# Optimization experiments

Hardware: AMD Instinct MI355X
Metric: run time of the kernel (lower is better)

## Reference

```python
import jax, jax.numpy as jnp
from jax import lax
import numpy as np


def _conv1d(x, w, b):
    # x: (N, C, L), w: (O, I, K), stride 2, padding 1 -> matches nn.Conv1d(k=4, s=2, p=1)
    y = lax.conv_general_dilated(x, w, window_strides=(2,), padding=[(1, 1)],
                                 dimension_numbers=('NCH', 'OIH', 'NCH'))
    return y + b[None, :, None]


def setup_inputs() -> dict:
    key = jax.random.key(0)
    k = jax.random.split(key, 6)
    B, C_in, T = 32, 256, 2048
    H, D, K_codes = 1024, 512, 1024
    s = 0.02
    return {
        'x': jax.random.normal(k[0], (B, C_in, T), dtype=jnp.float32),
        'w1': jax.random.normal(k[1], (H, C_in, 4), dtype=jnp.float32) * s,
        'b1': jnp.zeros((H,), dtype=jnp.float32),
        'w2': jax.random.normal(k[2], (D, H, 4), dtype=jnp.float32) * s,
        'b2': jnp.zeros((D,), dtype=jnp.float32),
        'codebook': jax.random.normal(k[3], (K_codes, D), dtype=jnp.float32) * s,
    }


def reference(x, w1, b1, w2, b2, codebook):
    z_e = _conv1d(jax.nn.relu(_conv1d(x, w1, b1)), w2, b2)  # (B, D, T/4)
    B, D, T = z_e.shape
    flat = z_e.transpose(0, 2, 1).reshape(-1, D)  # (B*T, D)
    # squared Euclidean distance; argmin identical to cdist(p=2) argmin
    d2 = (jnp.sum(flat * flat, axis=1, keepdims=True)
          - 2.0 * flat @ codebook.T
          + jnp.sum(codebook * codebook, axis=1)[None, :])  # (B*T, K)
    encoding_indices = jnp.argmin(d2, axis=1)  # (B*T,)
    # NOTE: faithful to the original .view(z_e.shape) (a raw reshape, no permute back)
    z_q = codebook[encoding_indices].reshape(B, D, T)
    return (z_q, encoding_indices, z_e)
```

## Files before the change

kernel.cpp:

```cpp
#include <hip/hip_runtime.h>
#include <hip/hip_bf16.h>

using f16x8 = __attribute__((ext_vector_type(8))) _Float16;
using f32x4 = __attribute__((ext_vector_type(4))) float;

union PackU { unsigned u; _Float16 h[2]; };

__device__ inline unsigned split_pack(float v) {
    _Float16 h0 = (_Float16)v;
    float r = (v - (float)h0) * 4096.0f;
    PackU p; p.h[0] = h0; p.h[1] = (_Float16)r;
    return p.u;
}

__global__ __launch_bounds__(256) void split_kernel(const float* __restrict__ src,
                                                    unsigned* __restrict__ dst, int n4) {
    int g = blockIdx.x * 256 + threadIdx.x;
    if (g >= n4) return;
    float4 v = reinterpret_cast<const float4*>(src)[g];
    uint4 o;
    o.x = split_pack(v.x); o.y = split_pack(v.y);
    o.z = split_pack(v.z); o.w = split_pack(v.w);
    reinterpret_cast<uint4*>(dst)[g] = o;
}

#define BMt 128
#define BNt 128
#define BKt 32

__global__ __launch_bounds__(256, 2) void mfma_gemm(
    const unsigned* __restrict__ Ap, const unsigned* __restrict__ Bp,
    const float* __restrict__ bias,
    unsigned* __restrict__ OutP, float* __restrict__ OutF,
    int M, int N, int KK, int Cc, int L, int Lout, int LoutSh,
    int gatherMode, int mode)
{
    __shared__ uint4 As4[BMt * 8];
    __shared__ uint4 Bs4[BNt * 8];

    const int tid = threadIdx.x;
    const int m0 = blockIdx.y * BMt;
    const int n0 = blockIdx.x * BNt;

    const int srow = tid >> 1;
    const int kh = tid & 1;
    const int am = m0 + srow;
    const int ab = am >> LoutSh;
    const int at = am & (Lout - 1);
    const unsigned* aprow = Ap + (size_t)ab * Cc * L;
    const int ai0 = 2 * at - 1;
    const unsigned* adir = Ap + (size_t)am * KK;
    const unsigned* brow = Bp + (size_t)(n0 + srow) * KK;

    const int lane = tid & 63;
    const int wv = tid >> 6;
    const int wr = wv >> 1, wc = wv & 1;
    const int l15 = lane & 15, lq = lane >> 4;

    f32x4 acc0[4][4] = {{{0.f}}};
    f32x4 acc1[4][4] = {{{0.f}}};

    for (int k0 = 0; k0 < KK; k0 += BKt) {
        uint4 pa[4], pb[4];
        if (gatherMode) {
            int cbase = (k0 >> 2) + kh * 4;
#pragma unroll
            for (int cl = 0; cl < 4; cl++) {
                const unsigned* base = aprow + (size_t)(cbase + cl) * L;
                unsigned q0 = 0, q3 = 0;
                if (ai0 >= 0) q0 = base[ai0];
                unsigned q1 = base[ai0 + 1];
                unsigned q2 = base[ai0 + 2];
                if (ai0 + 3 < L) q3 = base[ai0 + 3];
                pa[cl].x = q0; pa[cl].y = q1; pa[cl].z = q2; pa[cl].w = q3;
            }
        } else {
            const uint4* s = reinterpret_cast<const uint4*>(adir + k0 + kh * 16);
            pa[0] = s[0]; pa[1] = s[1]; pa[2] = s[2]; pa[3] = s[3];
        }
        {
            const uint4* s = reinterpret_cast<const uint4*>(brow + k0 + kh * 16);
            pb[0] = s[0]; pb[1] = s[1]; pb[2] = s[2]; pb[3] = s[3];
        }

        __syncthreads();

#pragma unroll
        for (int ch = 0; ch < 2; ch++) {
            uint4 w0, w1, v0, v1;
            unsigned* W0 = (unsigned*)&w0; unsigned* W1 = (unsigned*)&w1;
            unsigned* V0 = (unsigned*)&v0; unsigned* V1 = (unsigned*)&v1;
#pragma unroll
            for (int j = 0; j < 4; j++) {
                int e0 = ch * 8 + 2 * j, e1 = e0 + 1;
                unsigned lo = ((const unsigned*)&pa[e0 >> 2])[e0 & 3];
                unsigned hi = ((const unsigned*)&pa[e1 >> 2])[e1 & 3];
                W0[j] = (lo & 0xffffu) | (hi << 16);
                W1[j] = (lo >> 16) | (hi & 0xffff0000u);
                lo = ((const unsigned*)&pb[e0 >> 2])[e0 & 3];
                hi = ((const unsigned*)&pb[e1 >> 2])[e1 & 3];
                V0[j] = (lo & 0xffffu) | (hi << 16);
                V1[j] = (lo >> 16) | (hi & 0xffff0000u);
            }
            int kc = kh * 2 + ch;
            int sw = srow & 7;
            As4[srow * 8 + ((kc) ^ sw)] = w0;
            As4[srow * 8 + ((4 + kc) ^ sw)] = w1;
            Bs4[srow * 8 + ((kc) ^ sw)] = v0;
            Bs4[srow * 8 + ((4 + kc) ^ sw)] = v1;
        }

        __syncthreads();

        f16x8 a0f[4], a1f[4], b0f[4], b1f[4];
#pragma unroll
        for (int mf = 0; mf < 4; mf++) {
            int row = wr * 64 + mf * 16 + l15;
            int sw = row & 7;
            a0f[mf] = *reinterpret_cast<const f16x8*>(&As4[row * 8 + (lq ^ sw)]);
            a1f[mf] = *reinterpret_cast<const f16x8*>(&As4[row * 8 + ((4 + lq) ^ sw)]);
        }
#pragma unroll
        for (int nf = 0; nf < 4; nf++) {
            int row = wc * 64 + nf * 16 + l15;
            int sw = row & 7;
            b0f[nf] = *reinterpret_cast<const f16x8*>(&Bs4[row * 8 + (lq ^ sw)]);
            b1f[nf] = *reinterpret_cast<const f16x8*>(&Bs4[row * 8 + ((4 + lq) ^ sw)]);
        }
#pragma unroll
        for (int mf = 0; mf < 4; mf++)
#pragma unroll
            for (int nf = 0; nf < 4; nf++) {
                acc0[mf][nf] = __builtin_amdgcn_mfma_f32_16x16x32_f16(
                    a0f[mf], b0f[nf], acc0[mf][nf], 0, 0, 0);
                acc1[mf][nf] = __builtin_amdgcn_mfma_f32_16x16x32_f16(
                    a0f[mf], b1f[nf], acc1[mf][nf], 0, 0, 0);
                acc1[mf][nf] = __builtin_amdgcn_mfma_f32_16x16x32_f16(
                    a1f[mf], b0f[nf], acc1[mf][nf], 0, 0, 0);
            }
    }

    const float s12 = 1.0f / 4096.0f;
    const int LoutM = Lout - 1;

    if (mode == 2) {
#pragma unroll
        for (int mf = 0; mf < 4; mf++) {
            int mb = m0 + wr * 64 + mf * 16 + lq * 4;
#pragma unroll
            for (int nf = 0; nf < 4; nf++) {
                int n = n0 + wc * 64 + nf * 16 + l15;
#pragma unroll
                for (int r = 0; r < 4; r++) {
                    float v = acc0[mf][nf][r] + acc1[mf][nf][r] * s12;
                    OutF[(size_t)(mb + r) * N + n] = v;
                }
            }
        }
    } else if (mode == 0) {
#pragma unroll
        for (int mf = 0; mf < 4; mf++) {
            int mb = m0 + wr * 64 + mf * 16 + lq * 4;
            int b = mb >> LoutSh, t = mb & LoutM;
#pragma unroll
            for (int nf = 0; nf < 4; nf++) {
                int n = n0 + wc * 64 + nf * 16 + l15;
                float bv = bias[n];
                uint4 o;
                unsigned* O = (unsigned*)&o;
#pragma unroll
                for (int r = 0; r < 4; r++) {
                    float v = acc0[mf][nf][r] + acc1[mf][nf][r] * s12 + bv;
                    v = fmaxf(v, 0.f);
                    O[r] = split_pack(v);
                }
                *reinterpret_cast<uint4*>(&OutP[((size_t)b * N + n) * Lout + t]) = o;
            }
        }
    } else {
#pragma unroll
        for (int mf = 0; mf < 4; mf++) {
            int mb = m0 + wr * 64 + mf * 16 + lq * 4;
            int b = mb >> LoutSh, t = mb & LoutM;
#pragma unroll
            for (int nf = 0; nf < 4; nf++) {
                int n = n0 + wc * 64 + nf * 16 + l15;
                float bv = bias[n];
                float4 f;
                unsigned O[4];
#pragma unroll
                for (int r = 0; r < 4; r++) {
                    float v = acc0[mf][nf][r] + acc1[mf][nf][r] * s12 + bv;
                    ((float*)&f)[r] = v;
                    O[r] = split_pack(v);
                }
                *reinterpret_cast<float4*>(&OutF[((size_t)b * N + n) * Lout + t]) = f;
#pragma unroll
                for (int r = 0; r < 4; r++)
                    OutP[(size_t)(mb + r) * N + n] = O[r];
            }
        }
    }
}

__global__ __launch_bounds__(64) void cb_norm(const float* __restrict__ cb,
                                              float* __restrict__ cn2) {
    int n = blockIdx.x;
    int lane = threadIdx.x;
    float s = 0.f;
    for (int d = lane; d < 512; d += 64) {
        float v = cb[(size_t)n * 512 + d];
        s += v * v;
    }
#pragma unroll
    for (int off = 32; off; off >>= 1) s += __shfl_down(s, off);
    if (lane == 0) cn2[n] = s;
}

__global__ __launch_bounds__(256) void argmin_k(const float* __restrict__ S,
                                                const float* __restrict__ cn2,
                                                float* __restrict__ idxf,
                                                int* __restrict__ idxi, int rows) {
    int wid = threadIdx.x >> 6;
    int lane = threadIdx.x & 63;
    int r = blockIdx.x * 4 + wid;
    if (r >= rows) return;
    const float* srow = S + (size_t)r * 1024;
    float best = INFINITY;
    int bi = 0;
#pragma unroll
    for (int it = 0; it < 4; it++) {
        int nb = it * 256 + lane * 4;
        float4 s4 = *reinterpret_cast<const float4*>(&srow[nb]);
        float4 c4 = *reinterpret_cast<const float4*>(&cn2[nb]);
        float v;
        v = c4.x - 2.f * s4.x; if (v < best) { best = v; bi = nb + 0; }
        v = c4.y - 2.f * s4.y; if (v < best) { best = v; bi = nb + 1; }
        v = c4.z - 2.f * s4.z; if (v < best) { best = v; bi = nb + 2; }
        v = c4.w - 2.f * s4.w; if (v < best) { best = v; bi = nb + 3; }
    }
#pragma unroll
    for (int off = 32; off; off >>= 1) {
        float ov = __shfl_down(best, off);
        int oi = __shfl_down(bi, off);
        if (ov < best || (ov == best && oi < bi)) { best = ov; bi = oi; }
    }
    if (lane == 0) {
        idxf[r] = (float)bi;
        idxi[r] = bi;
    }
}

__global__ __launch_bounds__(256) void gather_k(const int* __restrict__ idx,
                                                const float* __restrict__ cb,
                                                float* __restrict__ zq, int total4) {
    int g = blockIdx.x * 256 + threadIdx.x;
    if (g >= total4) return;
    int r = g >> 7;
    int d4 = g & 127;
    int id = idx[r];
    *reinterpret_cast<float4*>(&zq[(size_t)r * 512 + (size_t)d4 * 4]) =
        *reinterpret_cast<const float4*>(&cb[(size_t)id * 512 + (size_t)d4 * 4]);
}

extern "C" void kernel_launch(void* const* d_in, const int* in_sizes, int n_in,
                              void* d_out, int out_size, void* d_ws, size_t ws_size,
                              hipStream_t stream) {
    const float* x  = (const float*)d_in[0];
    const float* w1 = (const float*)d_in[1];
    const float* b1 = (const float*)d_in[2];
    const float* w2 = (const float*)d_in[3];
    const float* b2 = (const float*)d_in[4];
    const float* cb = (const float*)d_in[5];
    float* out = (float*)d_out;

    const int B = 32, Cin = 256, T = 2048, H = 1024, D = 512, Kc = 1024;
    const int T1 = 1024, T2 = 512;

    float* zq_out  = out;
    float* idx_out = out + (size_t)B * T2 * D;
    float* ze_out  = idx_out + (size_t)B * T2;

    unsigned* w1p = (unsigned*)d_ws;
    unsigned* w2p = w1p + (size_t)H * Cin * 4;
    unsigned* cbp = w2p + (size_t)D * H * 4;
    float* cn2    = (float*)(cbp + (size_t)Kc * D);
    int* idx_ws   = (int*)(cn2 + Kc);
    unsigned* dyn = (unsigned*)(idx_ws + B * T2);

    size_t fixed_u32 = (size_t)H * Cin * 4 + (size_t)D * H * 4 + (size_t)Kc * D
                       + Kc + (size_t)B * T2 + 256;
    int NB = 32;
    while (NB > 1 &&
           (fixed_u32 + (size_t)NB * ((size_t)Cin * T + (size_t)H * T1 + (size_t)T2 * D))
               * 4 > ws_size)
        NB >>= 1;

    unsigned* xp = dyn;
    unsigned* hp = xp + (size_t)NB * Cin * T;
    unsigned* zp = hp + (size_t)NB * H * T1;
    float* S = (float*)hp;

    split_kernel<<<(H * Cin * 4 / 4 + 255) / 256, 256, 0, stream>>>(w1, w1p, H * Cin * 4 / 4);
    split_kernel<<<(D * H * 4 / 4 + 255) / 256, 256, 0, stream>>>(w2, w2p, D * H * 4 / 4);
    split_kernel<<<(Kc * D / 4 + 255) / 256, 256, 0, stream>>>(cb, cbp, Kc * D / 4);
    cb_norm<<<Kc, 64, 0, stream>>>(cb, cn2);

    for (int b0 = 0; b0 < B; b0 += NB) {
        int nb = (B - b0 < NB) ? (B - b0) : NB;

        split_kernel<<<(nb * Cin * T / 4 + 255) / 256, 256, 0, stream>>>(
            x + (size_t)b0 * Cin * T, xp, nb * Cin * T / 4);

        mfma_gemm<<<dim3(H / BNt, nb * T1 / BMt), 256, 0, stream>>>(
            xp, w1p, b1, hp, nullptr,
            nb * T1, H, Cin * 4, Cin, T, T1, 10, 1, 0);

        mfma_gemm<<<dim3(D / BNt, nb * T2 / BMt), 256, 0, stream>>>(
            hp, w2p, b2, zp, ze_out + (size_t)b0 * D * T2,
            nb * T2, D, H * 4, H, T1, T2, 9, 1, 1);

        mfma_gemm<<<dim3(Kc / BNt, nb * T2 / BMt), 256, 0, stream>>>(
            zp, cbp, nullptr, nullptr, S,
            nb * T2, Kc, D, D, T2, T2, 9, 0, 2);

        argmin_k<<<(nb * T2 + 3) / 4, 256, 0, stream>>>(
            S, cn2, idx_out + (size_t)b0 * T2, idx_ws, nb * T2);

        gather_k<<<(nb * T2 * D / 4 + 255) / 256, 256, 0, stream>>>(
            idx_ws, cb, zq_out + (size_t)b0 * T2 * D, nb * T2 * D / 4);
    }
}
```

Baseline: 598.6 us.

## Split fp16 hi/lo into separate planes and prefetch next K tile

Stores the fp16 high and residual parts in separate planar buffers instead of interleaved 32-bit pairs. This lets the GEMM load tiles with wide vector loads and use byte permutes for the conv gather instead of per-element shuffling. It also prefetches the next K tile into registers while MFMAs run, changes the LDS swizzle, and reorders weight taps in split_w. The cost is extra workspace bookkeeping and more complex gather logic with edge masks, which risks subtle correctness issues.

```diff
diff --git a/kernel.cpp b/kernel.cpp
--- a/kernel.cpp
+++ b/kernel.cpp
@@ -3,54 +3,81 @@
 
 using f16x8 = __attribute__((ext_vector_type(8))) _Float16;
 using f32x4 = __attribute__((ext_vector_type(4))) float;
-
-union PackU { unsigned u; _Float16 h[2]; };
-
-__device__ inline unsigned split_pack(float v) {
-    _Float16 h0 = (_Float16)v;
-    float r = (v - (float)h0) * 4096.0f;
-    PackU p; p.h[0] = h0; p.h[1] = (_Float16)r;
-    return p.u;
-}
-
-__global__ __launch_bounds__(256) void split_kernel(const float* __restrict__ src,
-                                                    unsigned* __restrict__ dst, int n4) {
+typedef unsigned uint4a __attribute__((ext_vector_type(4), aligned(4)));
+
+__device__ inline void sp2(float v, unsigned short& h0, unsigned short& h1) {
+    _Float16 a = (_Float16)v;
+    float r = (v - (float)a) * 4096.0f;
+    _Float16 b = (_Float16)r;
+    union { _Float16 f; unsigned short u; } c0, c1;
+    c0.f = a; c1.f = b;
+    h0 = c0.u; h1 = c1.u;
+}
+
+__global__ __launch_bounds__(256) void split_planes(const float* __restrict__ src,
+        ushort* __restrict__ p0, ushort* __restrict__ p1, int n4) {
     int g = blockIdx.x * 256 + threadIdx.x;
     if (g >= n4) return;
     float4 v = reinterpret_cast<const float4*>(src)[g];
-    uint4 o;
-    o.x = split_pack(v.x); o.y = split_pack(v.y);
-    o.z = split_pack(v.z); o.w = split_pack(v.w);
-    reinterpret_cast<uint4*>(dst)[g] = o;
-}
-
-#define BMt 128
-#define BNt 128
-#define BKt 32
+    ushort4 a, b;
+    sp2(v.x, a.x, b.x); sp2(v.y, a.y, b.y);
+    sp2(v.z, a.z, b.z); sp2(v.w, a.w, b.w);
+    *reinterpret_cast<ushort4*>(&p0[(size_t)g * 4]) = a;
+    *reinterpret_cast<ushort4*>(&p1[(size_t)g * 4]) = b;
+}
+
+__global__ __launch_bounds__(256) void split_w(const float* __restrict__ w,
+        ushort* __restrict__ p0, ushort* __restrict__ p1, int total) {
+    int g = blockIdx.x * 256 + threadIdx.x;
+    if (g >= total) return;
+    float4 v = reinterpret_cast<const float4*>(w)[g];
+    ushort4 a, b;
+    sp2(v.y, a.x, b.x);
+    sp2(v.z, a.y, b.y);
+    sp2(v.x, a.z, b.z);
+    sp2(v.w, a.w, b.w);
+    *reinterpret_cast<ushort4*>(&p0[(size_t)g * 4]) = a;
+    *reinterpret_cast<ushort4*>(&p1[(size_t)g * 4]) = b;
+}
 
 __global__ __launch_bounds__(256, 2) void mfma_gemm(
-    const unsigned* __restrict__ Ap, const unsigned* __restrict__ Bp,
+    const ushort* __restrict__ A0, const ushort* __restrict__ A1,
+    const ushort* __restrict__ B0, const ushort* __restrict__ B1,
     const float* __restrict__ bias,
-    unsigned* __restrict__ OutP, float* __restrict__ OutF,
+    ushort* __restrict__ OP0, ushort* __restrict__ OP1,
+    float* __restrict__ OutF,
     int M, int N, int KK, int Cc, int L, int Lout, int LoutSh,
     int gatherMode, int mode)
 {
-    __shared__ uint4 As4[BMt * 8];
-    __shared__ uint4 Bs4[BNt * 8];
+    __shared__ uint4 As4[128 * 8];
+    __shared__ uint4 Bs4[128 * 8];
 
     const int tid = threadIdx.x;
-    const int m0 = blockIdx.y * BMt;
-    const int n0 = blockIdx.x * BNt;
+    const int m0 = blockIdx.y * 128;
+    const int n0 = blockIdx.x * 128;
 
     const int srow = tid >> 1;
     const int kh = tid & 1;
+    const int sw_s = (srow ^ (srow >> 3)) & 7;
+
     const int am = m0 + srow;
     const int ab = am >> LoutSh;
     const int at = am & (Lout - 1);
-    const unsigned* aprow = Ap + (size_t)ab * Cc * L;
-    const int ai0 = 2 * at - 1;
-    const unsigned* adir = Ap + (size_t)am * KK;
-    const unsigned* brow = Bp + (size_t)(n0 + srow) * KK;
+
+    const ushort* ag0 = nullptr;
+    const ushort* ag1 = nullptr;
+    const ushort* ad = nullptr;
+    unsigned bmask = 0xffffffffu;
+    if (gatherMode) {
+        long long off = (long long)ab * Cc * L + 2 * at - 2;
+        ag0 = A0 + off;
+        ag1 = A1 + off;
+        if (at == 0) bmask &= 0xffff0000u;
+        if (at == Lout - 1) bmask &= 0x0000ffffu;
+    } else {
+        ad = (kh ? A1 : A0) + (size_t)am * KK;
+    }
+    const ushort* bd = (kh ? B1 : B0) + (size_t)(n0 + srow) * KK;
 
     const int lane = tid & 63;
     const int wv = tid >> 6;
@@ -60,84 +87,85 @@
     f32x4 acc0[4][4] = {{{0.f}}};
     f32x4 acc1[4][4] = {{{0.f}}};
 
-    for (int k0 = 0; k0 < KK; k0 += BKt) {
-        uint4 pa[4], pb[4];
+    uint4 aw[4], bw[4];
+
+    auto loadA = [&](int k0) {
         if (gatherMode) {
-            int cbase = (k0 >> 2) + kh * 4;
-#pragma unroll
-            for (int cl = 0; cl < 4; cl++) {
-                const unsigned* base = aprow + (size_t)(cbase + cl) * L;
-                unsigned q0 = 0, q3 = 0;
-                if (ai0 >= 0) q0 = base[ai0];
-                unsigned q1 = base[ai0 + 1];
-                unsigned q2 = base[ai0 + 2];
-                if (ai0 + 3 < L) q3 = base[ai0 + 3];
-                pa[cl].x = q0; pa[cl].y = q1; pa[cl].z = q2; pa[cl].w = q3;
+            int cb_ = (k0 >> 2) + kh * 4;
+#pragma unroll
+            for (int q = 0; q < 2; q++) {
+                const ushort* l0 = ag0 + (size_t)(cb_ + 2 * q) * L;
+                const ushort* l1 = ag0 + (size_t)(cb_ + 2 * q + 1) * L;
+                const ushort* l2 = ag1 + (size_t)(cb_ + 2 * q) * L;
+                const ushort* l3 = ag1 + (size_t)(cb_ + 2 * q + 1) * L;
+                uint4a x0 = *(const uint4a*)l0;
+                uint4a x1 = *(const uint4a*)l1;
+                uint4a x2 = *(const uint4a*)l2;
+                uint4a x3 = *(const uint4a*)l3;
+                aw[q].x = x0.y;
+                aw[q].y = __builtin_amdgcn_perm(x0.z, x0.x, 0x05040302u) & bmask;
+                aw[q].z = x1.y;
+                aw[q].w = __builtin_amdgcn_perm(x1.z, x1.x, 0x05040302u) & bmask;
+                aw[2 + q].x = x2.y;
+                aw[2 + q].y = __builtin_amdgcn_perm(x2.z, x2.x, 0x05040302u) & bmask;
+                aw[2 + q].z = x3.y;
+                aw[2 + q].w = __builtin_amdgcn_perm(x3.z, x3.x, 0x05040302u) & bmask;
             }
         } else {
-            const uint4* s = reinterpret_cast<const uint4*>(adir + k0 + kh * 16);
-            pa[0] = s[0]; pa[1] = s[1]; pa[2] = s[2]; pa[3] = s[3];
-        }
-        {
-            const uint4* s = reinterpret_cast<const uint4*>(brow + k0 + kh * 16);
-            pb[0] = s[0]; pb[1] = s[1]; pb[2] = s[2]; pb[3] = s[3];
-        }
-
+#pragma unroll
+            for (int q = 0; q < 4; q++)
+                aw[q] = *reinterpret_cast<const uint4*>(ad + k0 + q * 8);
+        }
+    };
+    auto loadB = [&](int k0) {
+#pragma unroll
+        for (int q = 0; q < 4; q++)
+            bw[q] = *reinterpret_cast<const uint4*>(bd + k0 + q * 8);
+    };
+
+    loadA(0);
+    loadB(0);
+
+    for (int k0 = 0; k0 < KK; k0 += 32) {
         __syncthreads();
-
-#pragma unroll
-        for (int ch = 0; ch < 2; ch++) {
-            uint4 w0, w1, v0, v1;
-            unsigned* W0 = (unsigned*)&w0; unsigned* W1 = (unsigned*)&w1;
-            unsigned* V0 = (unsigned*)&v0; unsigned* V1 = (unsigned*)&v1;
-#pragma unroll
-            for (int j = 0; j < 4; j++) {
-                int e0 = ch * 8 + 2 * j, e1 = e0 + 1;
-                unsigned lo = ((const unsigned*)&pa[e0 >> 2])[e0 & 3];
-                unsigned hi = ((const unsigned*)&pa[e1 >> 2])[e1 & 3];
-                W0[j] = (lo & 0xffffu) | (hi << 16);
-                W1[j] = (lo >> 16) | (hi & 0xffff0000u);
-                lo = ((const unsigned*)&pb[e0 >> 2])[e0 & 3];
-                hi = ((const unsigned*)&pb[e1 >> 2])[e1 & 3];
-                V0[j] = (lo & 0xffffu) | (hi << 16);
-                V1[j] = (lo >> 16) | (hi & 0xffff0000u);
-            }
-            int kc = kh * 2 + ch;
-            int sw = srow & 7;
-            As4[srow * 8 + ((kc) ^ sw)] = w0;
-            As4[srow * 8 + ((4 + kc) ^ sw)] = w1;
-            Bs4[srow * 8 + ((kc) ^ sw)] = v0;
-            Bs4[srow * 8 + ((4 + kc) ^ sw)] = v1;
-        }
-
+        if (gatherMode) {
+            As4[srow * 8 + ((2 * kh + 0) ^ sw_s)] = aw[0];
+            As4[srow * 8 + ((2 * kh + 1) ^ sw_s)] = aw[1];
+            As4[srow * 8 + ((4 + 2 * kh + 0) ^ sw_s)] = aw[2];
+            As4[srow * 8 + ((4 + 2 * kh + 1) ^ sw_s)] = aw[3];
+        } else {
+#pragma unroll
+            for (int q = 0; q < 4; q++)
+                As4[srow * 8 + ((4 * kh + q) ^ sw_s)] = aw[q];
+        }
+#pragma unroll
+        for (int q = 0; q < 4; q++)
+            Bs4[srow * 8 + ((4 * kh + q) ^ sw_s)] = bw[q];
         __syncthreads();
 
-        f16x8 a0f[4], a1f[4], b0f[4], b1f[4];
+        if (k0 + 32 < KK) { loadA(k0 + 32); loadB(k0 + 32); }
+
+        f16x8 a0f[4], a1f[4];
 #pragma unroll
         for (int mf = 0; mf < 4; mf++) {
             int row = wr * 64 + mf * 16 + l15;
-            int sw = row & 7;
+            int sw = (row ^ (row >> 3)) & 7;
             a0f[mf] = *reinterpret_cast<const f16x8*>(&As4[row * 8 + (lq ^ sw)]);
             a1f[mf] = *reinterpret_cast<const f16x8*>(&As4[row * 8 + ((4 + lq) ^ sw)]);
         }
 #pragma unroll
         for (int nf = 0; nf < 4; nf++) {
             int row = wc * 64 + nf * 16 + l15;
-            int sw = row & 7;
-            b0f[nf] = *reinterpret_cast<const f16x8*>(&Bs4[row * 8 + (lq ^ sw)]);
-            b1f[nf] = *reinterpret_cast<const f16x8*>(&Bs4[row * 8 + ((4 + lq) ^ sw)]);
-        }
-#pragma unroll
-        for (int mf = 0; mf < 4; mf++)
-#pragma unroll
-            for (int nf = 0; nf < 4; nf++) {
-                acc0[mf][nf] = __builtin_amdgcn_mfma_f32_16x16x32_f16(
-                    a0f[mf], b0f[nf], acc0[mf][nf], 0, 0, 0);
-                acc1[mf][nf] = __builtin_amdgcn_mfma_f32_16x16x32_f16(
-                    a0f[mf], b1f[nf], acc1[mf][nf], 0, 0, 0);
-                acc1[mf][nf] = __builtin_amdgcn_mfma_f32_16x16x32_f16(
-                    a1f[mf], b0f[nf], acc1[mf][nf], 0, 0, 0);
-            }
+            int sw = (row ^ (row >> 3)) & 7;
+            f16x8 b0f = *reinterpret_cast<const f16x8*>(&Bs4[row * 8 + (lq ^ sw)]);
+            f16x8 b1f = *reinterpret_cast<const f16x8*>(&Bs4[row * 8 + ((4 + lq) ^ sw)]);
+#pragma unroll
+            for (int mf = 0; mf < 4; mf++) {
+                acc0[mf][nf] = __builtin_amdgcn_mfma_f32_16x16x32_f16(a0f[mf], b0f, acc0[mf][nf], 0, 0, 0);
+                acc1[mf][nf] = __builtin_amdgcn_mfma_f32_16x16x32_f16(a0f[mf], b1f, acc1[mf][nf], 0, 0, 0);
+                acc1[mf][nf] = __builtin_amdgcn_mfma_f32_16x16x32_f16(a1f[mf], b0f, acc1[mf][nf], 0, 0, 0);
+            }
+        }
     }
 
     const float s12 = 1.0f / 4096.0f;
@@ -151,10 +179,8 @@
             for (int nf = 0; nf < 4; nf++) {
                 int n = n0 + wc * 64 + nf * 16 + l15;
 #pragma unroll
-                for (int r = 0; r < 4; r++) {
-                    float v = acc0[mf][nf][r] + acc1[mf][nf][r] * s12;
-                    OutF[(size_t)(mb + r) * N + n] = v;
-                }
+                for (int r = 0; r < 4; r++)
+                    OutF[(size_t)(mb + r) * N + n] = acc0[mf][nf][r] + acc1[mf][nf][r] * s12;
             }
         }
     } else if (mode == 0) {
@@ -166,15 +192,15 @@
             for (int nf = 0; nf < 4; nf++) {
                 int n = n0 + wc * 64 + nf * 16 + l15;
                 float bv = bias[n];
-                uint4 o;
-                unsigned* O = (unsigned*)&o;
-#pragma unroll
-                for (int r = 0; r < 4; r++) {
-                    float v = acc0[mf][nf][r] + acc1[mf][nf][r] * s12 + bv;
-                    v = fmaxf(v, 0.f);
-                    O[r] = split_pack(v);
-                }
-                *reinterpret_cast<uint4*>(&OutP[((size_t)b * N + n) * Lout + t]) = o;
+                ushort4 o0, o1;
+                float v;
+                v = fmaxf(acc0[mf][nf][0] + acc1[mf][nf][0] * s12 + bv, 0.f); sp2(v, o0.x, o1.x);
+                v = fmaxf(acc0[mf][nf][1] + acc1[mf][nf][1] * s12 + bv, 0.f); sp2(v, o0.y, o1.y);
+                v = fmaxf(acc0[mf][nf][2] + acc1[mf][nf][2] * s12 + bv, 0.f); sp2(v, o0.z, o1.z);
+                v = fmaxf(acc0[mf][nf][3] + acc1[mf][nf][3] * s12 + bv, 0.f); sp2(v, o0.w, o1.w);
+                size_t base = ((size_t)b * N + n) * Lout + t;
+                *reinterpret_cast<ushort4*>(&OP0[base]) = o0;
+                *reinterpret_cast<ushort4*>(&OP1[base]) = o1;
             }
         }
     } else {
@@ -187,17 +213,19 @@
                 int n = n0 + wc * 64 + nf * 16 + l15;
                 float bv = bias[n];
                 float4 f;
-                unsigned O[4];
+                unsigned short h0[4], h1[4];
 #pragma unroll
                 for (int r = 0; r < 4; r++) {
                     float v = acc0[mf][nf][r] + acc1[mf][nf][r] * s12 + bv;
                     ((float*)&f)[r] = v;
-                    O[r] = split_pack(v);
+                    sp2(v, h0[r], h1[r]);
                 }
                 *reinterpret_cast<float4*>(&OutF[((size_t)b * N + n) * Lout + t]) = f;
 #pragma unroll
-                for (int r = 0; r < 4; r++)
-                    OutP[(size_t)(mb + r) * N + n] = O[r];
+                for (int r = 0; r < 4; r++) {
+                    OP0[(size_t)(mb + r) * N + n] = h0[r];
+                    OP1[(size_t)(mb + r) * N + n] = h1[r];
+                }
             }
         }
     }
@@ -281,48 +309,60 @@
     float* idx_out = out + (size_t)B * T2 * D;
     float* ze_out  = idx_out + (size_t)B * T2;
 
-    unsigned* w1p = (unsigned*)d_ws;
-    unsigned* w2p = w1p + (size_t)H * Cin * 4;
-    unsigned* cbp = w2p + (size_t)D * H * 4;
-    float* cn2    = (float*)(cbp + (size_t)Kc * D);
-    int* idx_ws   = (int*)(cn2 + Kc);
-    unsigned* dyn = (unsigned*)(idx_ws + B * T2);
-
-    size_t fixed_u32 = (size_t)H * Cin * 4 + (size_t)D * H * 4 + (size_t)Kc * D
-                       + Kc + (size_t)B * T2 + 256;
+    ushort* wsb = (ushort*)d_ws;
+    size_t cur = 32;
+    auto alloc16 = [&](size_t n) {
+        ushort* p = wsb + cur;
+        cur += (n + 31) & ~(size_t)31;
+        return p;
+    };
+
+    ushort* w1p0 = alloc16((size_t)H * Cin * 4);
+    ushort* w1p1 = alloc16((size_t)H * Cin * 4);
+    ushort* w2p0 = alloc16((size_t)D * H * 4);
+    ushort* w2p1 = alloc16((size_t)D * H * 4);
+    ushort* cbp0 = alloc16((size_t)Kc * D);
+    ushort* cbp1 = alloc16((size_t)Kc * D);
+    float* cn2   = (float*)alloc16(2 * (size_t)Kc);
+    int* idx_ws  = (int*)alloc16(2 * (size_t)B * T2);
+
+    size_t fixed = cur;
     int NB = 32;
     while (NB > 1 &&
-           (fixed_u32 + (size_t)NB * ((size_t)Cin * T + (size_t)H * T1 + (size_t)T2 * D))
-               * 4 > ws_size)
+           (fixed + 2 * ((size_t)NB * Cin * T + (size_t)NB * H * T1 + (size_t)NB * T2 * D) + 128)
+               * 2 > ws_size)
         NB >>= 1;
 
-    unsigned* xp = dyn;
-    unsigned* hp = xp + (size_t)NB * Cin * T;
-    unsigned* zp = hp + (size_t)NB * H * T1;
-    float* S = (float*)hp;
-
-    split_kernel<<<(H * Cin * 4 / 4 + 255) / 256, 256, 0, stream>>>(w1, w1p, H * Cin * 4 / 4);
-    split_kernel<<<(D * H * 4 / 4 + 255) / 256, 256, 0, stream>>>(w2, w2p, D * H * 4 / 4);
-    split_kernel<<<(Kc * D / 4 + 255) / 256, 256, 0, stream>>>(cb, cbp, Kc * D / 4);
+    ushort* xp0 = alloc16(2 * (size_t)NB * Cin * T);
+    ushort* xp1 = xp0 + (size_t)NB * Cin * T;
+    ushort* hp0 = alloc16((size_t)NB * H * T1);
+    ushort* hp1 = alloc16((size_t)NB * H * T1);
+    ushort* zp0 = alloc16((size_t)NB * T2 * D);
+    ushort* zp1 = alloc16((size_t)NB * T2 * D);
+    float* S = (float*)xp0;
+
+    split_w<<<(H * Cin + 255) / 256, 256, 0, stream>>>(w1, w1p0, w1p1, H * Cin);
+    split_w<<<(D * H + 255) / 256, 256, 0, stream>>>(w2, w2p0, w2p1, D * H);
+    split_planes<<<(Kc * D / 4 + 255) / 256, 256, 0, stream>>>(cb, cbp0, cbp1, Kc * D / 4);
     cb_norm<<<Kc, 64, 0, stream>>>(cb, cn2);
 
     for (int b0 = 0; b0 < B; b0 += NB) {
         int nb = (B - b0 < NB) ? (B - b0) : NB;
 
-        split_kernel<<<(nb * Cin * T / 4 + 255) / 256, 256, 0, stream>>>(
-            x + (size_t)b0 * Cin * T, xp, nb * Cin * T / 4);
-
-        mfma_gemm<<<dim3(H / BNt, nb * T1 / BMt), 256, 0, stream>>>(
-            xp, w1p, b1, hp, nullptr,
+        split_planes<<<(nb * Cin * T / 4 + 255) / 256, 256, 0, stream>>>(
+            x + (size_t)b0 * Cin * T, xp0, xp1, nb * Cin * T / 4);
+
+        mfma_gemm<<<dim3(H / 128, nb * T1 / 128), 256, 0, stream>>>(
+            xp0, xp1, w1p0, w1p1, b1, hp0, hp1, nullptr,
             nb * T1, H, Cin * 4, Cin, T, T1, 10, 1, 0);
 
-        mfma_gemm<<<dim3(D / BNt, nb * T2 / BMt), 256, 0, stream>>>(
-            hp, w2p, b2, zp, ze_out + (size_t)b0 * D * T2,
+        mfma_gemm<<<dim3(D / 128, nb * T2 / 128), 256, 0, stream>>>(
+            hp0, hp1, w2p0, w2p1, b2, zp0, zp1, ze_out + (size_t)b0 * D * T2,
             nb * T2, D, H * 4, H, T1, T2, 9, 1, 1);
 
-        mfma_gemm<<<dim3(Kc / BNt, nb * T2 / BMt), 256, 0, stream>>>(
-            zp, cbp, nullptr, nullptr, S,
-            nb * T2, Kc, D, D, T2, T2, 9, 0, 2);
+        mfma_gemm<<<dim3(Kc / 128, nb * T2 / 128), 256, 0, stream>>>(
+            zp0, zp1, cbp0, cbp1, nullptr, nullptr, nullptr, S,
+            nb * T2, Kc, D, 0, 0, T2, 9, 0, 2);
 
         argmin_k<<<(nb * T2 + 3) / 4, 256, 0, stream>>>(
             S, cn2, idx_out + (size_t)b0 * T2, idx_ws, nb * T2);
```

Result: slower. 1.159 ms (+93.6%).

## Pre-split weights into hi/lo planes and register-prefetch next K tile in GEMM

Applied to the files above, without the earlier changes.

Weights and the codebook are now pre-split into separate high and low fp16 planes, so the GEMM can copy B tiles straight into shared memory without per-iteration repacking. The main loop loads the next K-slice of A and B into registers while the current slice's MFMAs run, giving software prefetch. A-operand repacking uses v_perm byte permutes, B fragments are loaded per nf inside the MFMA loop, and the grid is transposed so blockIdx.x walks M. This costs extra register pressure from the prefetch buffers, and the changed block order affects L2 reuse.

```diff
diff --git a/kernel.cpp b/kernel.cpp
--- a/kernel.cpp
+++ b/kernel.cpp
@@ -24,33 +24,47 @@
     reinterpret_cast<uint4*>(dst)[g] = o;
 }
 
-#define BMt 128
-#define BNt 128
-#define BKt 32
+__global__ __launch_bounds__(256) void split_planes(const float* __restrict__ src,
+        ushort* __restrict__ p0, ushort* __restrict__ p1, int n4) {
+    int g = blockIdx.x * 256 + threadIdx.x;
+    if (g >= n4) return;
+    float4 v = reinterpret_cast<const float4*>(src)[g];
+    ushort4 a, b;
+    unsigned u;
+    u = split_pack(v.x); a.x = (ushort)u; b.x = (ushort)(u >> 16);
+    u = split_pack(v.y); a.y = (ushort)u; b.y = (ushort)(u >> 16);
+    u = split_pack(v.z); a.z = (ushort)u; b.z = (ushort)(u >> 16);
+    u = split_pack(v.w); a.w = (ushort)u; b.w = (ushort)(u >> 16);
+    *reinterpret_cast<ushort4*>(&p0[(size_t)g * 4]) = a;
+    *reinterpret_cast<ushort4*>(&p1[(size_t)g * 4]) = b;
+}
 
 __global__ __launch_bounds__(256, 2) void mfma_gemm(
-    const unsigned* __restrict__ Ap, const unsigned* __restrict__ Bp,
+    const unsigned* __restrict__ Ap,
+    const ushort* __restrict__ B0, const ushort* __restrict__ B1,
     const float* __restrict__ bias,
     unsigned* __restrict__ OutP, float* __restrict__ OutF,
     int M, int N, int KK, int Cc, int L, int Lout, int LoutSh,
     int gatherMode, int mode)
 {
-    __shared__ uint4 As4[BMt * 8];
-    __shared__ uint4 Bs4[BNt * 8];
+    __shared__ uint4 As4[128 * 8];
+    __shared__ uint4 Bs4[128 * 8];
 
     const int tid = threadIdx.x;
-    const int m0 = blockIdx.y * BMt;
-    const int n0 = blockIdx.x * BNt;
+    const int m0 = blockIdx.x * 128;
+    const int n0 = blockIdx.y * 128;
 
     const int srow = tid >> 1;
     const int kh = tid & 1;
+    const int sw_s = srow & 7;
+
     const int am = m0 + srow;
     const int ab = am >> LoutSh;
     const int at = am & (Lout - 1);
     const unsigned* aprow = Ap + (size_t)ab * Cc * L;
     const int ai0 = 2 * at - 1;
     const unsigned* adir = Ap + (size_t)am * KK;
-    const unsigned* brow = Bp + (size_t)(n0 + srow) * KK;
+    const ushort* bd = (kh ? B1 : B0) + (size_t)(n0 + srow) * KK;
 
     const int lane = tid & 63;
     const int wv = tid >> 6;
@@ -60,8 +74,9 @@
     f32x4 acc0[4][4] = {{{0.f}}};
     f32x4 acc1[4][4] = {{{0.f}}};
 
-    for (int k0 = 0; k0 < KK; k0 += BKt) {
-        uint4 pa[4], pb[4];
+    uint4 pa[4], bw[4];
+
+    auto loadA = [&](int k0) {
         if (gatherMode) {
             int cbase = (k0 >> 2) + kh * 4;
 #pragma unroll
@@ -76,43 +91,47 @@
             }
         } else {
             const uint4* s = reinterpret_cast<const uint4*>(adir + k0 + kh * 16);
-            pa[0] = s[0]; pa[1] = s[1]; pa[2] = s[2]; pa[3] = s[3];
-        }
-        {
-            const uint4* s = reinterpret_cast<const uint4*>(brow + k0 + kh * 16);
-            pb[0] = s[0]; pb[1] = s[1]; pb[2] = s[2]; pb[3] = s[3];
-        }
-
+#pragma unroll
+            for (int q = 0; q < 4; q++) pa[q] = s[q];
+        }
+    };
+    auto loadB = [&](int k0) {
+#pragma unroll
+        for (int q = 0; q < 4; q++)
+            bw[q] = *reinterpret_cast<const uint4*>(bd + k0 + q * 8);
+    };
+
+    loadA(0);
+    loadB(0);
+
+    for (int k0 = 0; k0 < KK; k0 += 32) {
         __syncthreads();
 
 #pragma unroll
+        for (int q = 0; q < 4; q++)
+            Bs4[srow * 8 + ((4 * kh + q) ^ sw_s)] = bw[q];
+
+#pragma unroll
         for (int ch = 0; ch < 2; ch++) {
-            uint4 w0, w1, v0, v1;
+            uint4 w0, w1;
             unsigned* W0 = (unsigned*)&w0; unsigned* W1 = (unsigned*)&w1;
-            unsigned* V0 = (unsigned*)&v0; unsigned* V1 = (unsigned*)&v1;
 #pragma unroll
             for (int j = 0; j < 4; j++) {
                 int e0 = ch * 8 + 2 * j, e1 = e0 + 1;
                 unsigned lo = ((const unsigned*)&pa[e0 >> 2])[e0 & 3];
                 unsigned hi = ((const unsigned*)&pa[e1 >> 2])[e1 & 3];
-                W0[j] = (lo & 0xffffu) | (hi << 16);
-                W1[j] = (lo >> 16) | (hi & 0xffff0000u);
-                lo = ((const unsigned*)&pb[e0 >> 2])[e0 & 3];
-                hi = ((const unsigned*)&pb[e1 >> 2])[e1 & 3];
-                V0[j] = (lo & 0xffffu) | (hi << 16);
-                V1[j] = (lo >> 16) | (hi & 0xffff0000u);
+                W0[j] = __builtin_amdgcn_perm(hi, lo, 0x05040100u);
+                W1[j] = __builtin_amdgcn_perm(hi, lo, 0x07060302u);
             }
             int kc = kh * 2 + ch;
-            int sw = srow & 7;
-            As4[srow * 8 + ((kc) ^ sw)] = w0;
-            As4[srow * 8 + ((4 + kc) ^ sw)] = w1;
-            Bs4[srow * 8 + ((kc) ^ sw)] = v0;
-            Bs4[srow * 8 + ((4 + kc) ^ sw)] = v1;
-        }
-
+            As4[srow * 8 + (kc ^ sw_s)] = w0;
+            As4[srow * 8 + ((4 + kc) ^ sw_s)] = w1;
+        }
         __syncthreads();
 
-        f16x8 a0f[4], a1f[4], b0f[4], b1f[4];
+        if (k0 + 32 < KK) { loadA(k0 + 32); loadB(k0 + 32); }
+
+        f16x8 a0f[4], a1f[4];
 #pragma unroll
         for (int mf = 0; mf < 4; mf++) {
             int row = wr * 64 + mf * 16 + l15;
@@ -124,20 +143,15 @@
         for (int nf = 0; nf < 4; nf++) {
             int row = wc * 64 + nf * 16 + l15;
             int sw = row & 7;
-            b0f[nf] = *reinterpret_cast<const f16x8*>(&Bs4[row * 8 + (lq ^ sw)]);
-            b1f[nf] = *reinterpret_cast<const f16x8*>(&Bs4[row * 8 + ((4 + lq) ^ sw)]);
-        }
-#pragma unroll
-        for (int mf = 0; mf < 4; mf++)
-#pragma unroll
-            for (int nf = 0; nf < 4; nf++) {
-                acc0[mf][nf] = __builtin_amdgcn_mfma_f32_16x16x32_f16(
-                    a0f[mf], b0f[nf], acc0[mf][nf], 0, 0, 0);
-                acc1[mf][nf] = __builtin_amdgcn_mfma_f32_16x16x32_f16(
-                    a0f[mf], b1f[nf], acc1[mf][nf], 0, 0, 0);
-                acc1[mf][nf] = __builtin_amdgcn_mfma_f32_16x16x32_f16(
-                    a1f[mf], b0f[nf], acc1[mf][nf], 0, 0, 0);
-            }
+            f16x8 b0f = *reinterpret_cast<const f16x8*>(&Bs4[row * 8 + (lq ^ sw)]);
+            f16x8 b1f = *reinterpret_cast<const f16x8*>(&Bs4[row * 8 + ((4 + lq) ^ sw)]);
+#pragma unroll
+            for (int mf = 0; mf < 4; mf++) {
+                acc0[mf][nf] = __builtin_amdgcn_mfma_f32_16x16x32_f16(a0f[mf], b0f, acc0[mf][nf], 0, 0, 0);
+                acc1[mf][nf] = __builtin_amdgcn_mfma_f32_16x16x32_f16(a0f[mf], b1f, acc1[mf][nf], 0, 0, 0);
+                acc1[mf][nf] = __builtin_amdgcn_mfma_f32_16x16x32_f16(a1f[mf], b0f, acc1[mf][nf], 0, 0, 0);
+            }
+        }
     }
 
     const float s12 = 1.0f / 4096.0f;
@@ -151,10 +165,8 @@
             for (int nf = 0; nf < 4; nf++) {
                 int n = n0 + wc * 64 + nf * 16 + l15;
 #pragma unroll
-                for (int r = 0; r < 4; r++) {
-                    float v = acc0[mf][nf][r] + acc1[mf][nf][r] * s12;
-                    OutF[(size_t)(mb + r) * N + n] = v;
-                }
+                for (int r = 0; r < 4; r++)
+                    OutF[(size_t)(mb + r) * N + n] = acc0[mf][nf][r] + acc1[mf][nf][r] * s12;
             }
         }
     } else if (mode == 0) {
@@ -281,29 +293,38 @@
     float* idx_out = out + (size_t)B * T2 * D;
     float* ze_out  = idx_out + (size_t)B * T2;
 
-    unsigned* w1p = (unsigned*)d_ws;
-    unsigned* w2p = w1p + (size_t)H * Cin * 4;
-    unsigned* cbp = w2p + (size_t)D * H * 4;
-    float* cn2    = (float*)(cbp + (size_t)Kc * D);
-    int* idx_ws   = (int*)(cn2 + Kc);
-    unsigned* dyn = (unsigned*)(idx_ws + B * T2);
-
-    size_t fixed_u32 = (size_t)H * Cin * 4 + (size_t)D * H * 4 + (size_t)Kc * D
-                       + Kc + (size_t)B * T2 + 256;
+    unsigned* wsb = (unsigned*)d_ws;
+    size_t cur = 0;
+    auto alloc32 = [&](size_t n) {
+        unsigned* p = wsb + cur;
+        cur += (n + 15) & ~(size_t)15;
+        return p;
+    };
+
+    ushort* w1p0 = (ushort*)alloc32((size_t)H * Cin * 2);
+    ushort* w1p1 = (ushort*)alloc32((size_t)H * Cin * 2);
+    ushort* w2p0 = (ushort*)alloc32((size_t)D * H * 2);
+    ushort* w2p1 = (ushort*)alloc32((size_t)D * H * 2);
+    ushort* cbp0 = (ushort*)alloc32((size_t)Kc * D / 2);
+    ushort* cbp1 = (ushort*)alloc32((size_t)Kc * D / 2);
+    float* cn2   = (float*)alloc32(Kc);
+    int* idx_ws  = (int*)alloc32((size_t)B * T2);
+
+    size_t fixed = cur;
     int NB = 32;
     while (NB > 1 &&
-           (fixed_u32 + (size_t)NB * ((size_t)Cin * T + (size_t)H * T1 + (size_t)T2 * D))
+           (fixed + (size_t)NB * ((size_t)Cin * T + (size_t)H * T1 + (size_t)T2 * D) + 64)
                * 4 > ws_size)
         NB >>= 1;
 
-    unsigned* xp = dyn;
-    unsigned* hp = xp + (size_t)NB * Cin * T;
-    unsigned* zp = hp + (size_t)NB * H * T1;
+    unsigned* xp = alloc32((size_t)NB * Cin * T);
+    unsigned* hp = alloc32((size_t)NB * H * T1);
+    unsigned* zp = alloc32((size_t)NB * T2 * D);
     float* S = (float*)hp;
 
-    split_kernel<<<(H * Cin * 4 / 4 + 255) / 256, 256, 0, stream>>>(w1, w1p, H * Cin * 4 / 4);
-    split_kernel<<<(D * H * 4 / 4 + 255) / 256, 256, 0, stream>>>(w2, w2p, D * H * 4 / 4);
-    split_kernel<<<(Kc * D / 4 + 255) / 256, 256, 0, stream>>>(cb, cbp, Kc * D / 4);
+    split_planes<<<(H * Cin + 255) / 256, 256, 0, stream>>>(w1, w1p0, w1p1, H * Cin);
+    split_planes<<<(D * H + 255) / 256, 256, 0, stream>>>(w2, w2p0, w2p1, D * H);
+    split_planes<<<(Kc * D / 4 + 255) / 256, 256, 0, stream>>>(cb, cbp0, cbp1, Kc * D / 4);
     cb_norm<<<Kc, 64, 0, stream>>>(cb, cn2);
 
     for (int b0 = 0; b0 < B; b0 += NB) {
@@ -312,17 +333,17 @@
         split_kernel<<<(nb * Cin * T / 4 + 255) / 256, 256, 0, stream>>>(
             x + (size_t)b0 * Cin * T, xp, nb * Cin * T / 4);
 
-        mfma_gemm<<<dim3(H / BNt, nb * T1 / BMt), 256, 0, stream>>>(
-            xp, w1p, b1, hp, nullptr,
+        mfma_gemm<<<dim3(nb * T1 / 128, H / 128), 256, 0, stream>>>(
+            xp, w1p0, w1p1, b1, hp, nullptr,
             nb * T1, H, Cin * 4, Cin, T, T1, 10, 1, 0);
 
-        mfma_gemm<<<dim3(D / BNt, nb * T2 / BMt), 256, 0, stream>>>(
-            hp, w2p, b2, zp, ze_out + (size_t)b0 * D * T2,
+        mfma_gemm<<<dim3(nb * T2 / 128, D / 128), 256, 0, stream>>>(
+            hp, w2p0, w2p1, b2, zp, ze_out + (size_t)b0 * D * T2,
             nb * T2, D, H * 4, H, T1, T2, 9, 1, 1);
 
-        mfma_gemm<<<dim3(Kc / BNt, nb * T2 / BMt), 256, 0, stream>>>(
-            zp, cbp, nullptr, nullptr, S,
-            nb * T2, Kc, D, D, T2, T2, 9, 0, 2);
+        mfma_gemm<<<dim3(nb * T2 / 128, Kc / 128), 256, 0, stream>>>(
+            zp, cbp0, cbp1, nullptr, nullptr, S,
+            nb * T2, Kc, D, 0, 0, T2, 9, 0, 2);
 
         argmin_k<<<(nb * T2 + 3) / 4, 256, 0, stream>>>(
             S, cn2, idx_out + (size_t)b0 * T2, idx_ws, nb * T2);
```

Measured after the change: 1.102 ms. 1.84x slower.
